# Kernel tuning notes

Measured on AMD Instinct MI355X. Metric: run time of the kernel, lower is better.

The kernel has to match this reference:

```python
import jax, jax.numpy as jnp
import numpy as np

DIM = 2048
DIM_HEAD = 64
NUM_HEADS = 32
FFN_INNER = 4 * DIM  # 8192
ATTN_INNER = NUM_HEADS * DIM_HEAD  # 2048
IN_WIDTH = FFN_INNER * 2 + 3 * ATTN_INNER  # 22528
OUT_IN = FFN_INNER + DIM  # 10240
B, S = 1, 2048


def setup_inputs() -> dict:
    key = jax.random.key(0)
    k0, k1, k2 = jax.random.split(key, 3)
    x = jax.random.normal(k0, (B, S, DIM), dtype=jnp.float32)
    W_in = jax.random.normal(k1, (DIM, IN_WIDTH), dtype=jnp.float32) * (DIM ** -0.5)
    W_out = jax.random.normal(k2, (OUT_IN, DIM), dtype=jnp.float32) * (OUT_IN ** -0.5)
    ln_w = jnp.ones((DIM,), dtype=jnp.float32)
    ln_b = jnp.zeros((DIM,), dtype=jnp.float32)
    return {"x": x, "ln_w": ln_w, "ln_b": ln_b, "W_in": W_in, "W_out": W_out}


def _layernorm(x, w, b, eps=1e-5):
    mu = jnp.mean(x, axis=-1, keepdims=True)
    var = jnp.mean(jnp.square(x - mu), axis=-1, keepdims=True)
    return (x - mu) * jax.lax.rsqrt(var + eps) * w + b


def reference(x, ln_w, ln_b, W_in, W_out):
    b, s, _ = x.shape
    h = _layernorm(x, ln_w, ln_b)
    res = h @ W_in  # [b, s, IN_WIDTH]
    q = res[..., :ATTN_INNER]
    k = res[..., ATTN_INNER:2 * ATTN_INNER]
    v = res[..., 2 * ATTN_INNER:3 * ATTN_INNER]
    ffn_input = res[..., 3 * ATTN_INNER:3 * ATTN_INNER + FFN_INNER]
    # b s (h d) -> b h s d
    q = q.reshape(b, s, NUM_HEADS, DIM_HEAD).transpose(0, 2, 1, 3)
    k = k.reshape(b, s, NUM_HEADS, DIM_HEAD).transpose(0, 2, 1, 3)
    v = v.reshape(b, s, NUM_HEADS, DIM_HEAD).transpose(0, 2, 1, 3)
    q = q * (DIM_HEAD ** -0.5)
    sim = jnp.einsum('bhsd,bhnd->bhsn', q, k)  # [b, h, s, s]
    causal = jnp.triu(jnp.ones((s, s), dtype=bool), k=1)
    sim = jnp.where(causal, -jnp.finfo(sim.dtype).max, sim)
    attn = jax.nn.softmax(sim, axis=-1)
    attn_out = jnp.einsum('bhsn,bhnd->bhsd', attn, v)
    attn_out = attn_out.transpose(0, 2, 1, 3).reshape(b, s, ATTN_INNER)
    concat_input = jnp.concatenate([attn_out, ffn_input], axis=-1)  # [b, s, OUT_IN]
    return concat_input @ W_out
```

## Files before the change

kernel.cpp:

```cpp
#include <hip/hip_runtime.h>
#include <stdint.h>

typedef __bf16 bf16x8 __attribute__((ext_vector_type(8)));
typedef float f32x4 __attribute__((ext_vector_type(4)));
typedef uint16_t u16x4 __attribute__((ext_vector_type(4)));
typedef uint16_t u16x8 __attribute__((ext_vector_type(8)));

#define LOG2E 1.4426950408889634f

__device__ __forceinline__ uint16_t f2bf(float f) {
  union { float f; uint32_t u; } v; v.f = f;
  return (uint16_t)((v.u + 0x7fffu + ((v.u >> 16) & 1u)) >> 16);
}

__device__ __forceinline__ void gload_lds16(const void* g, void* l) {
  __builtin_amdgcn_global_load_lds(
      (const __attribute__((address_space(1))) void*)g,
      (__attribute__((address_space(3))) void*)l, 16, 0, 0);
}

__device__ __forceinline__ f32x4 mfma16(bf16x8 a, bf16x8 b, f32x4 c) {
  return __builtin_amdgcn_mfma_f32_16x16x32_bf16(a, b, c, 0, 0, 0);
}

__global__ __launch_bounds__(256) void ln_kernel(const float* __restrict__ x,
                                                 const float* __restrict__ g,
                                                 const float* __restrict__ bta,
                                                 uint16_t* __restrict__ h) {
  const int row = blockIdx.x;
  const int t = threadIdx.x;
  const float* xr = x + (size_t)row * 2048 + t * 8;
  float4 v0 = *(const float4*)xr;
  float4 v1 = *(const float4*)(xr + 4);
  float s = v0.x + v0.y + v0.z + v0.w + v1.x + v1.y + v1.z + v1.w;
  float q = v0.x*v0.x + v0.y*v0.y + v0.z*v0.z + v0.w*v0.w
          + v1.x*v1.x + v1.y*v1.y + v1.z*v1.z + v1.w*v1.w;
  #pragma unroll
  for (int m = 1; m < 64; m <<= 1) {
    s += __shfl_xor(s, m);
    q += __shfl_xor(q, m);
  }
  __shared__ float ps[4], pq[4];
  const int wid = t >> 6, lane = t & 63;
  if (lane == 0) { ps[wid] = s; pq[wid] = q; }
  __syncthreads();
  s = ps[0] + ps[1] + ps[2] + ps[3];
  q = pq[0] + pq[1] + pq[2] + pq[3];
  const float mu = s * (1.0f / 2048.0f);
  const float var = q * (1.0f / 2048.0f) - mu * mu;
  const float rs = rsqrtf(var + 1e-5f);
  float4 w0 = *(const float4*)(g + t * 8);
  float4 w1 = *(const float4*)(g + t * 8 + 4);
  float4 b0 = *(const float4*)(bta + t * 8);
  float4 b1 = *(const float4*)(bta + t * 8 + 4);
  u16x8 o;
  o[0] = f2bf((v0.x - mu) * rs * w0.x + b0.x);
  o[1] = f2bf((v0.y - mu) * rs * w0.y + b0.y);
  o[2] = f2bf((v0.z - mu) * rs * w0.z + b0.z);
  o[3] = f2bf((v0.w - mu) * rs * w0.w + b0.w);
  o[4] = f2bf((v1.x - mu) * rs * w1.x + b1.x);
  o[5] = f2bf((v1.y - mu) * rs * w1.y + b1.y);
  o[6] = f2bf((v1.z - mu) * rs * w1.z + b1.z);
  o[7] = f2bf((v1.w - mu) * rs * w1.w + b1.w);
  *(u16x8*)(h + (size_t)row * 2048 + t * 8) = o;
}

__global__ __launch_bounds__(256) void transpose_w(const float* __restrict__ in,
                                                   uint16_t* __restrict__ out,
                                                   int R, int ldin,
                                                   int scale_cols, float scale) {
  __shared__ uint16_t tile[64][65];
  const int c0 = blockIdx.x * 64;
  const int r0 = blockIdx.y * 64;
  const int t = threadIdx.x;
  const int cc = (t & 15) * 4;
  const int rb = t >> 4;
  #pragma unroll
  for (int p = 0; p < 4; ++p) {
    const int r = rb + p * 16;
    const float4 v = *(const float4*)(in + (size_t)(r0 + r) * ldin + c0 + cc);
    const float m0 = (c0 + cc + 0) < scale_cols ? scale : 1.0f;
    const float m1 = (c0 + cc + 1) < scale_cols ? scale : 1.0f;
    const float m2 = (c0 + cc + 2) < scale_cols ? scale : 1.0f;
    const float m3 = (c0 + cc + 3) < scale_cols ? scale : 1.0f;
    tile[r][cc + 0] = f2bf(v.x * m0);
    tile[r][cc + 1] = f2bf(v.y * m1);
    tile[r][cc + 2] = f2bf(v.z * m2);
    tile[r][cc + 3] = f2bf(v.w * m3);
  }
  __syncthreads();
  #pragma unroll
  for (int p = 0; p < 4; ++p) {
    const int oc = rb + p * 16;
    u16x4 ov;
    ov.x = tile[cc + 0][oc];
    ov.y = tile[cc + 1][oc];
    ov.z = tile[cc + 2][oc];
    ov.w = tile[cc + 3][oc];
    *(u16x4*)(out + (size_t)(c0 + oc) * R + r0 + cc) = ov;
  }
}

__global__ __launch_bounds__(256) void transpose_v(const uint16_t* __restrict__ res,
                                                   uint16_t* __restrict__ vt) {
  __shared__ uint16_t tile[64][65];
  const int c0 = blockIdx.x * 64;
  const int r0 = blockIdx.y * 64;
  const int t = threadIdx.x;
  const int cc = (t & 15) * 4;
  const int rb = t >> 4;
  #pragma unroll
  for (int p = 0; p < 4; ++p) {
    const int r = rb + p * 16;
    const u16x4 v = *(const u16x4*)(res + (size_t)(r0 + r) * 14336 + 4096 + c0 + cc);
    tile[r][cc + 0] = v.x;
    tile[r][cc + 1] = v.y;
    tile[r][cc + 2] = v.z;
    tile[r][cc + 3] = v.w;
  }
  __syncthreads();
  #pragma unroll
  for (int p = 0; p < 4; ++p) {
    const int oc = rb + p * 16;
    u16x4 ov;
    ov.x = tile[cc + 0][oc];
    ov.y = tile[cc + 1][oc];
    ov.z = tile[cc + 2][oc];
    ov.w = tile[cc + 3][oc];
    *(u16x4*)(vt + (size_t)(c0 + oc) * 2048 + r0 + cc) = ov;
  }
}

template <int CONCAT, int CF32>
__global__ __launch_bounds__(256, 2) void gemm_tb(
    const uint16_t* __restrict__ A0, const uint16_t* __restrict__ A1,
    const uint16_t* __restrict__ B, void* __restrict__ C0, void* __restrict__ C1,
    int ldbK, int ldc, int kchunk, int nt) {
  __shared__ __attribute__((aligned(16))) uint16_t Alds[2][256 * 32];
  __shared__ __attribute__((aligned(16))) uint16_t Blds[2][128 * 32];
  const int bid = blockIdx.x;
  const int qx = gridDim.x >> 3;
  const int wg = (bid & 7) * qx + (bid >> 3);
  const int m0 = (wg & 7) << 8;
  const int n0 = (wg >> 3) << 7;
  const int sk = blockIdx.y;
  const int k0 = sk * kchunk;
  const int t = threadIdx.x, wid = t >> 6, lane = t & 63;
  const int wr = wid >> 1, wc = wid & 1;

  f32x4 acc[8][4] = {};

  auto stage = [&](int tt) {
    const int kg = k0 + tt * 32;
    const uint16_t* As; int lda, kc;
    if (CONCAT && kg >= 2048) { As = A1; lda = 14336; kc = kg + 4096; }
    else                      { As = A0; lda = 2048;  kc = kg; }
    char* ab = (char*)Alds[tt & 1];
    char* bb = (char*)Blds[tt & 1];
    #pragma unroll
    for (int j = 0; j < 4; ++j) {
      const int ch = j * 256 + t;
      const int r = ch >> 2, s = ch & 3;
      gload_lds16(As + (size_t)(m0 + r) * lda + kc + ((s ^ ((r >> 1) & 3)) << 3),
                  ab + ch * 16);
    }
    #pragma unroll
    for (int j = 0; j < 2; ++j) {
      const int ch = j * 256 + t;
      const int r = ch >> 2, s = ch & 3;
      gload_lds16(B + (size_t)(n0 + r) * ldbK + kg + ((s ^ ((r >> 1) & 3)) << 3),
                  bb + ch * 16);
    }
  };

  stage(0);
  for (int tt = 0; tt < nt; ++tt) {
    const int buf = tt & 1;
    asm volatile("s_waitcnt vmcnt(0)" ::: "memory");
    __builtin_amdgcn_s_barrier();
    __builtin_amdgcn_sched_barrier(0);
    if (tt + 1 < nt) stage(tt + 1);
    const char* Ab = (const char*)Alds[buf];
    const char* Bb = (const char*)Blds[buf];
    bf16x8 bfr[4], af[8];
    #pragma unroll
    for (int n = 0; n < 4; ++n) {
      const int r = wc * 64 + n * 16 + (lane & 15);
      const int c = (lane >> 4) ^ ((r >> 1) & 3);
      bfr[n] = *(const bf16x8*)(Bb + r * 64 + c * 16);
    }
    #pragma unroll
    for (int m = 0; m < 8; ++m) {
      const int r = wr * 128 + m * 16 + (lane & 15);
      const int c = (lane >> 4) ^ ((r >> 1) & 3);
      af[m] = *(const bf16x8*)(Ab + r * 64 + c * 16);
    }
    #pragma unroll
    for (int m = 0; m < 8; ++m)
      #pragma unroll
      for (int n = 0; n < 4; ++n)
        acc[m][n] = mfma16(af[m], bfr[n], acc[m][n]);
    __builtin_amdgcn_sched_barrier(0);
  }

  #pragma unroll
  for (int m = 0; m < 8; ++m)
    #pragma unroll
    for (int n = 0; n < 4; ++n)
      #pragma unroll
      for (int r = 0; r < 4; ++r) {
        const int row = m0 + wr * 128 + m * 16 + (lane >> 4) * 4 + r;
        const int col = n0 + wc * 64 + n * 16 + (lane & 15);
        if (CF32) {
          float* C = (sk == 0) ? (float*)C0
                               : ((float*)C1 + (size_t)(sk - 1) * 4194304ull);
          C[(size_t)row * ldc + col] = acc[m][n][r];
        } else {
          ((uint16_t*)C0)[(size_t)row * ldc + col] = f2bf(acc[m][n][r]);
        }
      }
}

__global__ __launch_bounds__(256) void reduce_add3(float* __restrict__ out,
                                                   const float* __restrict__ p) {
  const size_t i = ((size_t)blockIdx.x * 256 + threadIdx.x) * 4;
  float4 a = *(const float4*)(out + i);
  const float4 b = *(const float4*)(p + i);
  const float4 c = *(const float4*)(p + 4194304 + i);
  const float4 d = *(const float4*)(p + 8388608 + i);
  a.x += b.x + c.x + d.x;
  a.y += b.y + c.y + d.y;
  a.z += b.z + c.z + d.z;
  a.w += b.w + c.w + d.w;
  *(float4*)(out + i) = a;
}

__global__ __launch_bounds__(256) void attn_kernel(const uint16_t* __restrict__ res,
                                                   const uint16_t* __restrict__ vt,
                                                   uint16_t* __restrict__ aout) {
  const int qt = blockIdx.x;
  const int hh = blockIdx.y;
  const int q0 = qt * 128;
  const int t = threadIdx.x, wid = t >> 6, lane = t & 63;
  const int qw = q0 + wid * 32;
  __shared__ uint16_t Klds[64 * 64];
  __shared__ uint16_t Vlds[64 * 64];
  __shared__ uint16_t Plds[4 * 32 * 64];
  char* pbase = (char*)Plds + wid * 4096;

  bf16x8 qf[2][2];
  #pragma unroll
  for (int m = 0; m < 2; ++m)
    #pragma unroll
    for (int ks = 0; ks < 2; ++ks)
      qf[m][ks] = *(const bf16x8*)(res + (size_t)(qw + m * 16 + (lane & 15)) * 14336
                                   + hh * 64 + ks * 32 + (lane >> 4) * 8);
  f32x4 O[2][4] = {};
  f32x4 mrun[2], lrun[2];
  #pragma unroll
  for (int m = 0; m < 2; ++m)
    #pragma unroll
    for (int r = 0; r < 4; ++r) { mrun[m][r] = -1e30f; lrun[m][r] = 0.0f; }

  const int nkt = qt * 2 + 2;
  for (int kt = 0; kt < nkt; ++kt) {
    const int k0 = kt * 64;
    __syncthreads();
    #pragma unroll
    for (int i = 0; i < 2; ++i) {
      const int o = (wid * 2 + i) * 1024 + lane * 16;
      const int row = o >> 7;
      const int slot = (o >> 4) & 7;
      const int col = (slot ^ (row & 7)) << 3;
      gload_lds16(res + (size_t)(k0 + row) * 14336 + 2048 + hh * 64 + col,
                  (char*)Klds + (wid * 2 + i) * 1024);
      gload_lds16(vt + (size_t)(hh * 64 + row) * 2048 + k0 + col,
                  (char*)Vlds + (wid * 2 + i) * 1024);
    }
    __syncthreads();
    if (k0 <= qw + 31) {
      f32x4 s[2][4] = {};
      #pragma unroll
      for (int ks = 0; ks < 2; ++ks) {
        bf16x8 kf[4];
        #pragma unroll
        for (int n = 0; n < 4; ++n) {
          const int row = n * 16 + (lane & 15);
          const int slot = (ks * 4 + (lane >> 4)) ^ (row & 7);
          kf[n] = *(const bf16x8*)((const char*)Klds + row * 128 + slot * 16);
        }
        #pragma unroll
        for (int m = 0; m < 2; ++m)
          #pragma unroll
          for (int n = 0; n < 4; ++n)
            s[m][n] = mfma16(qf[m][ks], kf[n], s[m][n]);
      }
      if (k0 + 63 > qw) {
        #pragma unroll
        for (int m = 0; m < 2; ++m)
          #pragma unroll
          for (int n = 0; n < 4; ++n)
            #pragma unroll
            for (int r = 0; r < 4; ++r) {
              const int key = k0 + n * 16 + (lane & 15);
              const int qr = qw + m * 16 + (lane >> 4) * 4 + r;
              if (key > qr) s[m][n][r] = -1e30f;
            }
      }
      #pragma unroll
      for (int m = 0; m < 2; ++m) {
        f32x4 tmax = s[m][0];
        #pragma unroll
        for (int n = 1; n < 4; ++n)
          #pragma unroll
          for (int r = 0; r < 4; ++r) tmax[r] = fmaxf(tmax[r], s[m][n][r]);
        #pragma unroll
        for (int msk = 1; msk < 16; msk <<= 1)
          #pragma unroll
          for (int r = 0; r < 4; ++r) tmax[r] = fmaxf(tmax[r], __shfl_xor(tmax[r], msk));
        f32x4 newm, sc;
        #pragma unroll
        for (int r = 0; r < 4; ++r) {
          newm[r] = fmaxf(mrun[m][r], tmax[r]);
          sc[r] = exp2f((mrun[m][r] - newm[r]) * LOG2E);
          mrun[m][r] = newm[r];
        }
        f32x4 psum;
        #pragma unroll
        for (int r = 0; r < 4; ++r) psum[r] = 0.0f;
        #pragma unroll
        for (int n = 0; n < 4; ++n)
          #pragma unroll
          for (int r = 0; r < 4; ++r) {
            const float p = exp2f((s[m][n][r] - newm[r]) * LOG2E);
            s[m][n][r] = p;
            psum[r] += p;
          }
        #pragma unroll
        for (int msk = 1; msk < 16; msk <<= 1)
          #pragma unroll
          for (int r = 0; r < 4; ++r) psum[r] += __shfl_xor(psum[r], msk);
        #pragma unroll
        for (int r = 0; r < 4; ++r) lrun[m][r] = lrun[m][r] * sc[r] + psum[r];
        #pragma unroll
        for (int d = 0; d < 4; ++d)
          #pragma unroll
          for (int r = 0; r < 4; ++r) O[m][d][r] *= sc[r];
        #pragma unroll
        for (int n = 0; n < 4; ++n)
          #pragma unroll
          for (int r = 0; r < 4; ++r) {
            const int prow = m * 16 + (lane >> 4) * 4 + r;
            const int pcol = n * 16 + (lane & 15);
            *(uint16_t*)(pbase + prow * 128 + (((pcol >> 3) ^ (prow & 7)) << 4)
                         + (pcol & 7) * 2) = f2bf(s[m][n][r]);
          }
      }
      asm volatile("s_waitcnt lgkmcnt(0)" ::: "memory");
      #pragma unroll
      for (int ks = 0; ks < 2; ++ks) {
        bf16x8 pa[2], vf[4];
        #pragma unroll
        for (int m = 0; m < 2; ++m) {
          const int row = m * 16 + (lane & 15);
          const int slot = (ks * 4 + (lane >> 4)) ^ (row & 7);
          pa[m] = *(const bf16x8*)(pbase + row * 128 + slot * 16);
        }
        #pragma unroll
        for (int d = 0; d < 4; ++d) {
          const int row = d * 16 + (lane & 15);
          const int slot = (ks * 4 + (lane >> 4)) ^ (row & 7);
          vf[d] = *(const bf16x8*)((const char*)Vlds + row * 128 + slot * 16);
        }
        #pragma unroll
        for (int m = 0; m < 2; ++m)
          #pragma unroll
          for (int d = 0; d < 4; ++d)
            O[m][d] = mfma16(pa[m], vf[d], O[m][d]);
      }
    }
  }
  #pragma unroll
  for (int m = 0; m < 2; ++m) {
    f32x4 inv;
    #pragma unroll
    for (int r = 0; r < 4; ++r) inv[r] = 1.0f / lrun[m][r];
    #pragma unroll
    for (int d = 0; d < 4; ++d)
      #pragma unroll
      for (int r = 0; r < 4; ++r) {
        const int row = qw + m * 16 + (lane >> 4) * 4 + r;
        const int col = hh * 64 + d * 16 + (lane & 15);
        aout[(size_t)row * 2048 + col] = f2bf(O[m][d][r] * inv[r]);
      }
  }
}

extern "C" void kernel_launch(void* const* d_in, const int* in_sizes, int n_in,
                              void* d_out, int out_size, void* d_ws, size_t ws_size,
                              hipStream_t stream) {
  (void)in_sizes; (void)n_in; (void)out_size;
  const float* x     = (const float*)d_in[0];
  const float* ln_w  = (const float*)d_in[1];
  const float* ln_b  = (const float*)d_in[2];
  const float* W_in  = (const float*)d_in[3];
  const float* W_out = (const float*)d_in[4];

  const size_t need = 184549376ull;
  if (ws_size < need) return;
  char* ws = (char*)d_ws;
  size_t off = 0;
  uint16_t* h     = (uint16_t*)(ws + off); off += (size_t)2048 * 2048 * 2;
  uint16_t* WtIn  = (uint16_t*)(ws + off); off += (size_t)14336 * 2048 * 2;
  uint16_t* WtOut = (uint16_t*)(ws + off); off += (size_t)2048 * 10240 * 2;
  uint16_t* res   = (uint16_t*)(ws + off); off += (size_t)2048 * 14336 * 2;
  uint16_t* vt    = (uint16_t*)(ws + off); off += (size_t)2048 * 2048 * 2;
  uint16_t* aout  = (uint16_t*)(ws + off);
  float* partials = (float*)ws;

  ln_kernel<<<2048, 256, 0, stream>>>(x, ln_w, ln_b, h);
  transpose_w<<<dim3(224, 32), 256, 0, stream>>>(W_in, WtIn, 2048, 22528, 2048, 0.125f);
  transpose_w<<<dim3(32, 160), 256, 0, stream>>>(W_out, WtOut, 10240, 2048, 0, 1.0f);
  gemm_tb<0, 0><<<dim3(896, 1), 256, 0, stream>>>(h, nullptr, WtIn, res, nullptr,
                                                  2048, 14336, 0, 64);
  transpose_v<<<dim3(32, 32), 256, 0, stream>>>(res, vt);
  attn_kernel<<<dim3(16, 32), 256, 0, stream>>>(res, vt, aout);
  gemm_tb<1, 1><<<dim3(128, 4), 256, 0, stream>>>(aout, res, WtOut, d_out, partials,
                                                  10240, 2048, 2560, 80);
  reduce_add3<<<4096, 256, 0, stream>>>((float*)d_out, partials);
}
```

Before: 454.1 us.

## Triple-buffer LDS staging in GEMM and attention to prefetch two tiles ahead

Both the GEMM and attention kernels move from double (or single) buffered LDS tiles to a three-slot ring. Loads for tile t+2 are issued while tile t is computed, and waits use partial vmcnt counts so the newest loads can stay in flight. The attention kernel drops its two __syncthreads per iteration in favour of one barrier and gets a launch-bounds occupancy hint. The cost is more LDS per block: the GEMM needs 72KB, which may lower occupancy, and the partial-wait accounting must match the number of loads issued per stage.

Measured after the change: 454.7 us. About the same (+0.1%).

```diff
diff --git a/kernel.cpp b/kernel.cpp
--- a/kernel.cpp
+++ b/kernel.cpp
@@ -132,12 +132,12 @@
 }
 
 template <int CONCAT, int CF32>
-__global__ __launch_bounds__(256, 2) void gemm_tb(
+__global__ __launch_bounds__(256, 2) void gemm_r3(
     const uint16_t* __restrict__ A0, const uint16_t* __restrict__ A1,
     const uint16_t* __restrict__ B, void* __restrict__ C0, void* __restrict__ C1,
     int ldbK, int ldc, int kchunk, int nt) {
-  __shared__ __attribute__((aligned(16))) uint16_t Alds[2][256 * 32];
-  __shared__ __attribute__((aligned(16))) uint16_t Blds[2][128 * 32];
+  __shared__ __attribute__((aligned(16))) uint16_t Alds[3][256 * 32];
+  __shared__ __attribute__((aligned(16))) uint16_t Blds[3][128 * 32];
   const int bid = blockIdx.x;
   const int qx = gridDim.x >> 3;
   const int wg = (bid & 7) * qx + (bid >> 3);
@@ -155,8 +155,8 @@
     const uint16_t* As; int lda, kc;
     if (CONCAT && kg >= 2048) { As = A1; lda = 14336; kc = kg + 4096; }
     else                      { As = A0; lda = 2048;  kc = kg; }
-    char* ab = (char*)Alds[tt & 1];
-    char* bb = (char*)Blds[tt & 1];
+    char* ab = (char*)Alds[tt % 3];
+    char* bb = (char*)Blds[tt % 3];
     #pragma unroll
     for (int j = 0; j < 4; ++j) {
       const int ch = j * 256 + t;
@@ -173,13 +173,14 @@
     }
   };
 
-  stage(0);
+  stage(0); stage(1);
   for (int tt = 0; tt < nt; ++tt) {
-    const int buf = tt & 1;
-    asm volatile("s_waitcnt vmcnt(0)" ::: "memory");
+    const int buf = tt % 3;
+    if (tt + 1 < nt) { asm volatile("s_waitcnt vmcnt(6)" ::: "memory"); }
+    else             { asm volatile("s_waitcnt vmcnt(0)" ::: "memory"); }
     __builtin_amdgcn_s_barrier();
     __builtin_amdgcn_sched_barrier(0);
-    if (tt + 1 < nt) stage(tt + 1);
+    if (tt + 2 < nt) stage(tt + 2);
     const char* Ab = (const char*)Alds[buf];
     const char* Bb = (const char*)Blds[buf];
     bf16x8 bfr[4], af[8];
@@ -235,17 +236,17 @@
   *(float4*)(out + i) = a;
 }
 
-__global__ __launch_bounds__(256) void attn_kernel(const uint16_t* __restrict__ res,
-                                                   const uint16_t* __restrict__ vt,
-                                                   uint16_t* __restrict__ aout) {
+__global__ __launch_bounds__(256, 2) void attn_kernel(const uint16_t* __restrict__ res,
+                                                      const uint16_t* __restrict__ vt,
+                                                      uint16_t* __restrict__ aout) {
   const int qt = blockIdx.x;
   const int hh = blockIdx.y;
   const int q0 = qt * 128;
   const int t = threadIdx.x, wid = t >> 6, lane = t & 63;
   const int qw = q0 + wid * 32;
-  __shared__ uint16_t Klds[64 * 64];
-  __shared__ uint16_t Vlds[64 * 64];
-  __shared__ uint16_t Plds[4 * 32 * 64];
+  __shared__ __attribute__((aligned(16))) uint16_t Klds[3][64 * 64];
+  __shared__ __attribute__((aligned(16))) uint16_t Vlds[3][64 * 64];
+  __shared__ __attribute__((aligned(16))) uint16_t Plds[4 * 32 * 64];
   char* pbase = (char*)Plds + wid * 4096;
 
   bf16x8 qf[2][2];
@@ -262,10 +263,10 @@
     #pragma unroll
     for (int r = 0; r < 4; ++r) { mrun[m][r] = -1e30f; lrun[m][r] = 0.0f; }
 
-  const int nkt = qt * 2 + 2;
-  for (int kt = 0; kt < nkt; ++kt) {
+  auto stageKV = [&](int kt) {
     const int k0 = kt * 64;
-    __syncthreads();
+    char* kb = (char*)Klds[kt % 3];
+    char* vb = (char*)Vlds[kt % 3];
     #pragma unroll
     for (int i = 0; i < 2; ++i) {
       const int o = (wid * 2 + i) * 1024 + lane * 16;
@@ -273,12 +274,25 @@
       const int slot = (o >> 4) & 7;
       const int col = (slot ^ (row & 7)) << 3;
       gload_lds16(res + (size_t)(k0 + row) * 14336 + 2048 + hh * 64 + col,
-                  (char*)Klds + (wid * 2 + i) * 1024);
+                  kb + (wid * 2 + i) * 1024);
       gload_lds16(vt + (size_t)(hh * 64 + row) * 2048 + k0 + col,
-                  (char*)Vlds + (wid * 2 + i) * 1024);
-    }
-    __syncthreads();
+                  vb + (wid * 2 + i) * 1024);
+    }
+  };
+
+  const int nkt = qt * 2 + 2;
+  stageKV(0);
+  if (1 < nkt) stageKV(1);
+  for (int kt = 0; kt < nkt; ++kt) {
+    const int k0 = kt * 64;
+    if (kt + 1 < nkt) { asm volatile("s_waitcnt vmcnt(4)" ::: "memory"); }
+    else              { asm volatile("s_waitcnt vmcnt(0)" ::: "memory"); }
+    __builtin_amdgcn_s_barrier();
+    __builtin_amdgcn_sched_barrier(0);
+    if (kt + 2 < nkt) stageKV(kt + 2);
     if (k0 <= qw + 31) {
+      const char* Kb = (const char*)Klds[kt % 3];
+      const char* Vb = (const char*)Vlds[kt % 3];
       f32x4 s[2][4] = {};
       #pragma unroll
       for (int ks = 0; ks < 2; ++ks) {
@@ -287,7 +301,7 @@
         for (int n = 0; n < 4; ++n) {
           const int row = n * 16 + (lane & 15);
           const int slot = (ks * 4 + (lane >> 4)) ^ (row & 7);
-          kf[n] = *(const bf16x8*)((const char*)Klds + row * 128 + slot * 16);
+          kf[n] = *(const bf16x8*)(Kb + row * 128 + slot * 16);
         }
         #pragma unroll
         for (int m = 0; m < 2; ++m)
@@ -357,6 +371,7 @@
           }
       }
       asm volatile("s_waitcnt lgkmcnt(0)" ::: "memory");
+      __builtin_amdgcn_sched_barrier(0);
       #pragma unroll
       for (int ks = 0; ks < 2; ++ks) {
         bf16x8 pa[2], vf[4];
@@ -370,7 +385,7 @@
         for (int d = 0; d < 4; ++d) {
           const int row = d * 16 + (lane & 15);
           const int slot = (ks * 4 + (lane >> 4)) ^ (row & 7);
-          vf[d] = *(const bf16x8*)((const char*)Vlds + row * 128 + slot * 16);
+          vf[d] = *(const bf16x8*)(Vb + row * 128 + slot * 16);
         }
         #pragma unroll
         for (int m = 0; m < 2; ++m)
@@ -421,11 +436,11 @@
   ln_kernel<<<2048, 256, 0, stream>>>(x, ln_w, ln_b, h);
   transpose_w<<<dim3(224, 32), 256, 0, stream>>>(W_in, WtIn, 2048, 22528, 2048, 0.125f);
   transpose_w<<<dim3(32, 160), 256, 0, stream>>>(W_out, WtOut, 10240, 2048, 0, 1.0f);
-  gemm_tb<0, 0><<<dim3(896, 1), 256, 0, stream>>>(h, nullptr, WtIn, res, nullptr,
+  gemm_r3<0, 0><<<dim3(896, 1), 256, 0, stream>>>(h, nullptr, WtIn, res, nullptr,
                                                   2048, 14336, 0, 64);
   transpose_v<<<dim3(32, 32), 256, 0, stream>>>(res, vt);
   attn_kernel<<<dim3(16, 32), 256, 0, stream>>>(res, vt, aout);
-  gemm_tb<1, 1><<<dim3(128, 4), 256, 0, stream>>>(aout, res, WtOut, d_out, partials,
+  gemm_r3<1, 1><<<dim3(128, 4), 256, 0, stream>>>(aout, res, WtOut, d_out, partials,
                                                   10240, 2048, 2560, 80);
   reduce_add3<<<4096, 256, 0, stream>>>((float*)d_out, partials);
 }
```
